# Kernel optimization log

Hardware: AMD Instinct MI355X
Metric: run time of the kernel (lower is better)

Reference implementation:

```python
import jax, jax.numpy as jnp
import numpy as np

INV_SCALE = 1.0 / (0.5 * 9)  # module's inv_scale_factor; qk is DIVIDED by this (i.e. * 4.5)


def setup_inputs() -> dict:
    key0 = jax.random.key(0)
    ks = jax.random.split(key0, 8)
    B, Sq, Sk, D, Dv = 8, 2048, 2048, 128, 256
    return {
        "query": jax.random.normal(ks[0], (B, Sq, D), dtype=jnp.float32),
        "key": jax.random.normal(ks[1], (B, Sk, D), dtype=jnp.float32),
        "value": jax.random.normal(ks[2], (B, Sk, Dv), dtype=jnp.float32),
        "mask": jax.random.normal(ks[3], (B, Sq, Sk), dtype=jnp.float32),
        # Linear weights stored torch-style as [out_features, in_features]
        "W0": jax.random.normal(ks[4], (D, D), dtype=jnp.float32) * (1.0 / np.sqrt(D)),
        "W1": jax.random.normal(ks[5], (D, D), dtype=jnp.float32) * (1.0 / np.sqrt(D)),
        "W2": jax.random.normal(ks[6], (D, Dv), dtype=jnp.float32) * (1.0 / np.sqrt(Dv)),
        "Wout": jax.random.normal(ks[7], (Dv, D), dtype=jnp.float32) * (1.0 / np.sqrt(D)),
    }


def reference(query, key, value, mask, W0, W1, W2, Wout):
    r1 = jnp.einsum("bqd,od->bqo", query, W0)          # [B,Sq,128]
    r2 = jnp.einsum("bkd,od->bko", key, W1)            # [B,Sk,128]
    r3 = jnp.einsum("bkv,ov->bko", value, W2)          # [B,Sk,128]
    qk = jnp.einsum("bqd,bkd->bqk", r1, r2)            # [B,Sq,Sk]
    scaled_qk = qk / INV_SCALE
    softmax_qk = jax.nn.softmax(scaled_qk, axis=-1)
    # dropout is identity in eval mode (deterministic reference)
    v1 = jnp.einsum("bqk,bko->bqo", softmax_qk, r3)    # [B,Sq,128]
    v2 = jnp.einsum("bqo,vo->bqv", v1, Wout)           # [B,Sq,256]
    output = v2 + jnp.einsum("bqk,bkv->bqv", mask, value)
    return output
```

## Files before the change

kernel.cpp:

```cpp
#include <hip/hip_runtime.h>
#include <cstdint>

typedef __attribute__((ext_vector_type(8))) __bf16 bf16x8;
typedef __attribute__((ext_vector_type(4))) __bf16 bf16x4;
typedef __attribute__((ext_vector_type(4))) float f32x4;

#define MFMA16(a, b, c) __builtin_amdgcn_mfma_f32_16x16x32_bf16((a), (b), (c), 0, 0, 0)
#define WAITV(N) asm volatile("s_waitcnt vmcnt(" #N ")" ::: "memory")

static constexpr int SEQ = 2048;
static constexpr int DV = 256;
static constexpr float QK_SCALE = 4.5f;

__device__ __forceinline__ bf16x4 cvt4(float4 v) {
    bf16x4 y;
    y[0] = (__bf16)v.x; y[1] = (__bf16)v.y; y[2] = (__bf16)v.z; y[3] = (__bf16)v.w;
    return y;
}

__device__ __forceinline__ void gl_lds16(const void* g, void* l) {
    __builtin_amdgcn_global_load_lds((const __attribute__((address_space(1))) uint32_t*)g,
                                     (__attribute__((address_space(3))) uint32_t*)l, 16, 0, 0);
}

template <int K, int TRANS>
__device__ __forceinline__ void proj_body(const float* __restrict__ X,
                                          const float* __restrict__ W,
                                          __bf16* __restrict__ out,
                                          float outScale, int m0, char* smem) {
    auto ldsX = (__bf16(*)[136])smem;
    auto ldsW = (__bf16(*)[136])(smem + 64 * 136 * 2);

    const int t = threadIdx.x;
    const int w = t >> 6, l = t & 63, lrow = l & 15, lq = l >> 4;

    f32x4 acc[8];
#pragma unroll
    for (int i = 0; i < 8; ++i) acc[i] = f32x4{0.f, 0.f, 0.f, 0.f};

#pragma unroll
    for (int kh = 0; kh < K / 128; ++kh) {
        if (kh) __syncthreads();
#pragma unroll
        for (int i = 0; i < 8; ++i) {
            int idx = t + i * 256;
            int r = idx >> 5, c4 = idx & 31;
            float4 v = *(const float4*)(X + (size_t)(m0 + r) * K + kh * 128 + c4 * 4);
            *(bf16x4*)&ldsX[r][c4 * 4] = cvt4(v);
        }
#pragma unroll
        for (int i = 0; i < 16; ++i) {
            int idx = t + i * 256;
            int r = idx >> 5, c4 = idx & 31;
            float4 v = *(const float4*)(W + (size_t)r * K + kh * 128 + c4 * 4);
            *(bf16x4*)&ldsW[r][c4 * 4] = cvt4(v);
        }
        __syncthreads();

        bf16x8 aA[4];
#pragma unroll
        for (int kc = 0; kc < 4; ++kc)
            aA[kc] = *(const bf16x8*)((const char*)&ldsX[w * 16 + lrow][0] + kc * 64 + lq * 16);
#pragma unroll
        for (int nt = 0; nt < 8; ++nt) {
#pragma unroll
            for (int kc = 0; kc < 4; ++kc) {
                bf16x8 bB = *(const bf16x8*)((const char*)&ldsW[nt * 16 + lrow][0] + kc * 64 + lq * 16);
                acc[nt] = MFMA16(aA[kc], bB, acc[nt]);
            }
        }
    }

#pragma unroll
    for (int nt = 0; nt < 8; ++nt) {
        if (TRANS) {
            int gm = m0 + w * 16 + lq * 4;
            int b = gm >> 11, s = gm & 2047;
            int col = nt * 16 + lrow;
            int kt = s >> 5, s32 = s & 31;
            int slot = (s32 >> 3) ^ ((col >> 1) & 3);
            bf16x4 y;
#pragma unroll
            for (int j = 0; j < 4; ++j) y[j] = (__bf16)(acc[nt][j] * outScale);
            *(bf16x4*)(out + (((size_t)b * 64 + kt) * 128 + col) * 32 + slot * 8 + (s32 & 7)) = y;
        } else {
#pragma unroll
            for (int j = 0; j < 4; ++j) {
                int gm = m0 + w * 16 + lq * 4 + j;
                int col = nt * 16 + lrow;
                out[(size_t)gm * 128 + col] = (__bf16)(acc[nt][j] * outScale);
            }
        }
    }
}

__device__ __forceinline__ void vt_body(const float* __restrict__ V,
                                        __bf16* __restrict__ vt, int wg, char* smem) {
    auto tile = (__bf16(*)[72])smem;
    const int t = threadIdx.x;
    const int b = wg >> 7, by = (wg >> 5) & 3, bxx = wg & 31;
    const int s0 = bxx * 64, v0 = by * 64;
#pragma unroll
    for (int i = 0; i < 4; ++i) {
        int idx = t + i * 256;
        int r = idx >> 4, c4 = idx & 15;
        float4 x = *(const float4*)(V + ((size_t)b * SEQ + s0 + r) * DV + v0 + c4 * 4);
        *(bf16x4*)&tile[r][c4 * 4] = cvt4(x);
    }
    __syncthreads();
#pragma unroll
    for (int i = 0; i < 4; ++i) {
        int idx = t + i * 256;
        int vv = idx >> 4, c4 = idx & 15;
        bf16x4 y;
        y[0] = tile[c4 * 4 + 0][vv]; y[1] = tile[c4 * 4 + 1][vv];
        y[2] = tile[c4 * 4 + 2][vv]; y[3] = tile[c4 * 4 + 3][vv];
        int v = v0 + vv;
        int kt = (s0 >> 5) + (c4 >> 3);
        int slot = ((c4 >> 1) & 3) ^ ((v >> 1) & 3);
        *(bf16x4*)(vt + (((size_t)b * 64 + kt) * 256 + v) * 32 + slot * 8 + (c4 & 1) * 4) = y;
    }
}

__global__ __launch_bounds__(256) void k_pre(const float* __restrict__ q,
                                             const float* __restrict__ k,
                                             const float* __restrict__ v,
                                             const float* __restrict__ W0,
                                             const float* __restrict__ W1,
                                             const float* __restrict__ W2,
                                             const float* __restrict__ Wout,
                                             __bf16* __restrict__ r1s,
                                             __bf16* __restrict__ r2b,
                                             __bf16* __restrict__ r3t,
                                             __bf16* __restrict__ vtb,
                                             __bf16* __restrict__ wob) {
    __shared__ __align__(16) char smem[52224];
    const int bx = blockIdx.x;
    if (bx < 256) {
        proj_body<128, 0>(q, W0, r1s, QK_SCALE, bx * 64, smem);
    } else if (bx < 512) {
        proj_body<128, 0>(k, W1, r2b, 1.0f, (bx - 256) * 64, smem);
    } else if (bx < 768) {
        proj_body<256, 1>(v, W2, r3t, 1.0f, (bx - 512) * 64, smem);
    } else if (bx < 1792) {
        vt_body(v, vtb, bx - 768, smem);
    } else {
        int i = (bx - 1792) * 256 + threadIdx.x;
        if (i < 8192) {
            float4 x = *(const float4*)(Wout + (size_t)i * 4);
            *(bf16x4*)(wob + (size_t)i * 4) = cvt4(x);
        }
    }
}

__global__ __launch_bounds__(256) void k_flash(const __bf16* __restrict__ r1s,
                                               const __bf16* __restrict__ r2,
                                               const __bf16* __restrict__ r3p,
                                               __bf16* __restrict__ v1p,
                                               float* __restrict__ ml) {
    __shared__ __align__(16) __bf16 r2s[4][32 * 128];
    __shared__ __align__(16) __bf16 r3s[4][128 * 32];
    __shared__ __bf16 plds[4][16][48];

    const int t = threadIdx.x;
    const int bx = (int)((blockIdx.x & 7) * 64 + (blockIdx.x >> 3));
    const int b = bx >> 6, rem = bx & 63, q0 = (rem >> 1) * 64, kh = rem & 1;
    const int w = t >> 6, l = t & 63, lrow = l & 15, lq = l >> 4;

    const __bf16* r1b = r1s + (size_t)b * SEQ * 128;
    const __bf16* r2b = r2 + (size_t)b * SEQ * 128 + (size_t)kh * 1024 * 128;
    const __bf16* r3b = r3p + (size_t)b * 64 * 128 * 32 + (size_t)kh * 32 * 128 * 32;

    bf16x8 aQ[4];
    {
        const __bf16* p = r1b + (size_t)(q0 + w * 16 + lrow) * 128 + lq * 8;
#pragma unroll
        for (int kc = 0; kc < 4; ++kc) aQ[kc] = *(const bf16x8*)(p + kc * 32);
    }

    const __bf16* p_r2[2];
    const __bf16* p_r3[2];
#pragma unroll
    for (int q1 = 0; q1 < 2; ++q1) {
        int r = 8 * w + 4 * q1 + (l >> 4);
        int c = (l & 15) ^ (r & 15);
        p_r2[q1] = r2b + (size_t)r * 128 + c * 8;
        p_r3[q1] = r3b + (size_t)(2 * w + q1) * 512 + l * 8;
    }

    auto stage = [&](int bi) {
#pragma unroll
        for (int q1 = 0; q1 < 2; ++q1) {
            gl_lds16(p_r2[q1], &r2s[bi][(2 * w + q1) * 512]);
            gl_lds16(p_r3[q1], &r3s[bi][(2 * w + q1) * 512]);
            p_r2[q1] += 32 * 128;
            p_r3[q1] += 128 * 32;
        }
    };

    f32x4 acc[8];
#pragma unroll
    for (int i = 0; i < 8; ++i) acc[i] = f32x4{0.f, 0.f, 0.f, 0.f};
    float mrow[4] = {-INFINITY, -INFINITY, -INFINITY, -INFINITY};
    float lsum[4] = {0.f, 0.f, 0.f, 0.f};

    stage(0); stage(1); stage(2);
    for (int it = 0; it < 32; ++it) {
        if (it < 30) { WAITV(8); } else if (it == 30) { WAITV(4); } else { WAITV(0); }
        __builtin_amdgcn_s_barrier();
        __builtin_amdgcn_sched_barrier(0);
        if (it + 3 < 32) stage((it + 3) & 3);
        __builtin_amdgcn_sched_barrier(0);
        const __bf16* R2 = &r2s[it & 3][0];
        const __bf16* R3 = &r3s[it & 3][0];

        f32x4 sc[2];
#pragma unroll
        for (int ct = 0; ct < 2; ++ct) {
            f32x4 s = f32x4{0.f, 0.f, 0.f, 0.f};
#pragma unroll
            for (int kc = 0; kc < 4; ++kc) {
                int p = (kc * 4 + lq) ^ lrow;
                bf16x8 bb = *(const bf16x8*)&R2[(ct * 16 + lrow) * 128 + p * 8];
                s = MFMA16(aQ[kc], bb, s);
            }
            sc[ct] = s;
        }

        float pm[4], al[4];
#pragma unroll
        for (int j = 0; j < 4; ++j) pm[j] = fmaxf(sc[0][j], sc[1][j]);
#pragma unroll
        for (int off = 1; off <= 8; off <<= 1)
#pragma unroll
            for (int j = 0; j < 4; ++j) pm[j] = fmaxf(pm[j], __shfl_xor(pm[j], off, 64));
#pragma unroll
        for (int j = 0; j < 4; ++j) {
            float mn = fmaxf(mrow[j], pm[j]);
            al[j] = __expf(mrow[j] - mn);
            mrow[j] = mn;
        }
        float pr[2][4];
#pragma unroll
        for (int ct = 0; ct < 2; ++ct)
#pragma unroll
            for (int j = 0; j < 4; ++j)
                pr[ct][j] = __expf(sc[ct][j] - mrow[j]);
#pragma unroll
        for (int j = 0; j < 4; ++j)
            lsum[j] = lsum[j] * al[j] + pr[0][j] + pr[1][j];
#pragma unroll
        for (int ot = 0; ot < 8; ++ot)
#pragma unroll
            for (int j = 0; j < 4; ++j) acc[ot][j] *= al[j];

#pragma unroll
        for (int ct = 0; ct < 2; ++ct)
#pragma unroll
            for (int j = 0; j < 4; ++j)
                plds[w][lq * 4 + j][ct * 16 + lrow] = (__bf16)pr[ct][j];
        __builtin_amdgcn_s_waitcnt(0xc07f);
        bf16x8 pA = *(const bf16x8*)&plds[w][lrow][lq * 8];

#pragma unroll
        for (int ot = 0; ot < 8; ++ot) {
            int p = lq ^ ((lrow >> 1) & 3);
            bf16x8 bb = *(const bf16x8*)&R3[(ot * 16 + lrow) * 32 + p * 8];
            acc[ot] = MFMA16(pA, bb, acc[ot]);
        }
    }

#pragma unroll
    for (int off = 1; off <= 8; off <<= 1)
#pragma unroll
        for (int j = 0; j < 4; ++j) lsum[j] += __shfl_xor(lsum[j], off, 64);

    __bf16* vp = v1p + (size_t)kh * 8 * SEQ * 128;
#pragma unroll
    for (int ot = 0; ot < 8; ++ot)
#pragma unroll
        for (int j = 0; j < 4; ++j) {
            int q = q0 + w * 16 + lq * 4 + j;
            float v = acc[ot][j] / lsum[j];
            vp[((size_t)b * SEQ + q) * 128 + ot * 16 + lrow] = (__bf16)v;
        }
    if (lrow == 0) {
#pragma unroll
        for (int j = 0; j < 4; ++j) {
            size_t row = (size_t)b * SEQ + q0 + w * 16 + lq * 4 + j;
            ml[((size_t)kh * 8 * SEQ + row) * 2 + 0] = mrow[j];
            ml[((size_t)kh * 8 * SEQ + row) * 2 + 1] = lsum[j];
        }
    }
}

__global__ __launch_bounds__(512, 4) void k_out(const float* __restrict__ mask,
                                                const __bf16* __restrict__ vtp,
                                                const __bf16* __restrict__ v1p,
                                                const float* __restrict__ ml,
                                                const __bf16* __restrict__ wob,
                                                float* __restrict__ out) {
    __shared__ __align__(16) __bf16 vbuf[3][256 * 32];
    __shared__ __align__(16) float mbuf[4][32 * 64];

    const int t = threadIdx.x;
    const int bid = (int)((blockIdx.x & 7) * 64 + (blockIdx.x >> 3));
    const int m0 = bid * 32;
    const int b = m0 >> 11, q0 = m0 & 2047;
    const int w = t >> 6, l = t & 63, lrow = l & 15, lq = l >> 4;
    const int rg = w & 1, cg = w >> 1;

    f32x4 acc[4];
#pragma unroll
    for (int i = 0; i < 4; ++i) acc[i] = f32x4{0.f, 0.f, 0.f, 0.f};

    const __bf16* vsrc[4];
    const float* msrc[2];
    if (w < 4) {
#pragma unroll
        for (int i = 0; i < 4; ++i)
            vsrc[i] = vtp + (size_t)b * 64 * 8192 + (w * 4 + i) * 512 + l * 8;
    } else {
        const int m = w - 4;
#pragma unroll
        for (int s = 0; s < 2; ++s) {
            int r = 4 * (m * 2 + s) + (l >> 4);
            int c = (l & 15) ^ (r & 7);
            msrc[s] = mask + ((size_t)(b * 2048 + q0 + r)) * 2048 + c * 4;
        }
    }

    if (w < 4) {
#pragma unroll
        for (int kt = 0; kt < 2; ++kt)
#pragma unroll
            for (int i = 0; i < 4; ++i)
                gl_lds16(vsrc[i] + (size_t)kt * 8192, &vbuf[kt][(w * 4 + i) * 512]);
    } else {
        const int m = w - 4;
#pragma unroll
        for (int e = 0; e < 2; ++e)
#pragma unroll
            for (int s = 0; s < 2; ++s)
                gl_lds16(msrc[s] + (size_t)e * 64, &mbuf[e][(m * 2 + s) * 256]);
    }

    for (int it = 0; it < 64; ++it) {
        if (w >= 4) {
            const int m = w - 4;
            if (it <= 59) {
                int en = (it >> 1) + 2, s = it & 1;
                gl_lds16(msrc[s] + (size_t)en * 64, &mbuf[en & 3][(m * 2 + s) * 256]);
            }
            if ((it & 1) == 0) {
                if (it <= 58) { WAITV(3); } else if (it == 60) { WAITV(2); } else { WAITV(0); }
            }
        } else {
            if (it < 63) { WAITV(4); } else { WAITV(0); }
        }
        __builtin_amdgcn_s_barrier();
        __builtin_amdgcn_sched_barrier(0);
        if (w < 4 && it + 2 < 64) {
            int kt = it + 2;
#pragma unroll
            for (int i = 0; i < 4; ++i)
                gl_lds16(vsrc[i] + (size_t)kt * 8192, &vbuf[kt % 3][(w * 4 + i) * 512]);
        }
        __builtin_amdgcn_sched_barrier(0);

        const float* Mb = &mbuf[(it >> 1) & 3][0];
        const __bf16* V = &vbuf[it % 3][0];
        const int h = it & 1;
        int c0 = (h * 8 + lq * 2) ^ (lrow & 7);
        int c1 = (h * 8 + lq * 2 + 1) ^ (lrow & 7);
        float4 f0 = *(const float4*)&Mb[(rg * 16 + lrow) * 64 + c0 * 4];
        float4 f1 = *(const float4*)&Mb[(rg * 16 + lrow) * 64 + c1 * 4];
        bf16x8 aM;
        aM[0] = (__bf16)f0.x; aM[1] = (__bf16)f0.y; aM[2] = (__bf16)f0.z; aM[3] = (__bf16)f0.w;
        aM[4] = (__bf16)f1.x; aM[5] = (__bf16)f1.y; aM[6] = (__bf16)f1.z; aM[7] = (__bf16)f1.w;

        const int pv = lq ^ ((lrow >> 1) & 3);
#pragma unroll
        for (int vt8 = 0; vt8 < 4; ++vt8) {
            bf16x8 bb = *(const bf16x8*)&V[(cg * 64 + vt8 * 16 + lrow) * 32 + pv * 8];
            acc[vt8] = MFMA16(aM, bb, acc[vt8]);
        }
    }

    const int NROW = 8 * SEQ;
    const int row = m0 + rg * 16 + lrow;
    float am0 = ml[(size_t)row * 2 + 0], al0 = ml[(size_t)row * 2 + 1];
    float am1 = ml[((size_t)NROW + row) * 2 + 0], al1 = ml[((size_t)NROW + row) * 2 + 1];
    float M = fmaxf(am0, am1);
    float w0 = al0 * __expf(am0 - M), w1 = al1 * __expf(am1 - M);
    float inv = 1.f / (w0 + w1);
    w0 *= inv; w1 *= inv;
    bf16x8 aV[4];
#pragma unroll
    for (int oc = 0; oc < 4; ++oc) {
        bf16x8 a = *(const bf16x8*)(v1p + (size_t)row * 128 + oc * 32 + lq * 8);
        bf16x8 bh = *(const bf16x8*)(v1p + ((size_t)NROW + row) * 128 + oc * 32 + lq * 8);
        bf16x8 o;
#pragma unroll
        for (int j = 0; j < 8; ++j) o[j] = (__bf16)((float)a[j] * w0 + (float)bh[j] * w1);
        aV[oc] = o;
    }
#pragma unroll
    for (int vt8 = 0; vt8 < 4; ++vt8) {
#pragma unroll
        for (int oc = 0; oc < 4; ++oc) {
            bf16x8 bb = *(const bf16x8*)(wob + (size_t)(cg * 64 + vt8 * 16 + lrow) * 128 + oc * 32 + lq * 8);
            acc[vt8] = MFMA16(aV[oc], bb, acc[vt8]);
        }
    }

#pragma unroll
    for (int vt8 = 0; vt8 < 4; ++vt8)
#pragma unroll
        for (int j = 0; j < 4; ++j) {
            int gq = m0 + rg * 16 + lq * 4 + j;
            out[(size_t)gq * 256 + cg * 64 + vt8 * 16 + lrow] = acc[vt8][j];
        }
}

extern "C" void kernel_launch(void* const* d_in, const int* in_sizes, int n_in,
                              void* d_out, int out_size, void* d_ws, size_t ws_size,
                              hipStream_t stream) {
    const float* q    = (const float*)d_in[0];
    const float* k    = (const float*)d_in[1];
    const float* v    = (const float*)d_in[2];
    const float* mask = (const float*)d_in[3];
    const float* W0   = (const float*)d_in[4];
    const float* W1   = (const float*)d_in[5];
    const float* W2   = (const float*)d_in[6];
    const float* Wout = (const float*)d_in[7];
    float* out = (float*)d_out;

    char* ws = (char*)d_ws;
    __bf16* r1s = (__bf16*)(ws);
    __bf16* r2b = (__bf16*)(ws + (4ull << 20));
    __bf16* r3t = (__bf16*)(ws + (8ull << 20));
    __bf16* vtb = (__bf16*)(ws + (12ull << 20));
    __bf16* wob = (__bf16*)(ws + (20ull << 20));
    __bf16* v1p = (__bf16*)(ws + (25ull << 20));
    float*  mlb = (float*)(ws + (33ull << 20));

    k_pre<<<1824, 256, 0, stream>>>(q, k, v, W0, W1, W2, Wout, r1s, r2b, r3t, vtb, wob);
    k_flash<<<512, 256, 0, stream>>>(r1s, r2b, r3t, v1p, mlb);
    k_out<<<512, 512, 0, stream>>>(mask, vtb, v1p, mlb, wob, out);
}
```

Before: 335.1 us.

## Pre-convert mask to bf16 in prep kernel and deepen V pipeline in output kernel

Adds a grid-stride section to the prep kernel that converts the full fp32 mask to bf16 in workspace. The output kernel then streams bf16 mask tiles into LDS and loads MFMA operands directly without per-iteration conversion, and the V tile ring grows from 3 to 4 stages with a prefetch distance of 3. The aim is to halve mask bytes and LDS use in the output GEMM and remove conversion ALU work. In exchange the mask is read in fp32 once and written and re-read in bf16, which adds total HBM traffic.

```diff
diff --git a/kernel.cpp b/kernel.cpp
--- a/kernel.cpp
+++ b/kernel.cpp
@@ -129,11 +129,13 @@
                                              const float* __restrict__ W1,
                                              const float* __restrict__ W2,
                                              const float* __restrict__ Wout,
+                                             const float* __restrict__ mask,
                                              __bf16* __restrict__ r1s,
                                              __bf16* __restrict__ r2b,
                                              __bf16* __restrict__ r3t,
                                              __bf16* __restrict__ vtb,
-                                             __bf16* __restrict__ wob) {
+                                             __bf16* __restrict__ wob,
+                                             __bf16* __restrict__ maskb) {
     __shared__ __align__(16) char smem[52224];
     const int bx = blockIdx.x;
     if (bx < 256) {
@@ -144,11 +146,23 @@
         proj_body<256, 1>(v, W2, r3t, 1.0f, (bx - 512) * 64, smem);
     } else if (bx < 1792) {
         vt_body(v, vtb, bx - 768, smem);
-    } else {
+    } else if (bx < 1824) {
         int i = (bx - 1792) * 256 + threadIdx.x;
         if (i < 8192) {
             float4 x = *(const float4*)(Wout + (size_t)i * 4);
             *(bf16x4*)(wob + (size_t)i * 4) = cvt4(x);
+        }
+    } else {
+        const size_t N = (size_t)8 * 2048 * 2048;
+        const size_t stride = (size_t)1024 * 256 * 8;
+        size_t i = ((size_t)(bx - 1824) * 256 + threadIdx.x) * 8;
+        for (; i < N; i += stride) {
+            float4 a = *(const float4*)(mask + i);
+            float4 b2 = *(const float4*)(mask + i + 4);
+            bf16x8 o;
+            o[0] = (__bf16)a.x; o[1] = (__bf16)a.y; o[2] = (__bf16)a.z; o[3] = (__bf16)a.w;
+            o[4] = (__bf16)b2.x; o[5] = (__bf16)b2.y; o[6] = (__bf16)b2.z; o[7] = (__bf16)b2.w;
+            *(bf16x8*)(maskb + i) = o;
         }
     }
 }
@@ -294,14 +308,14 @@
     }
 }
 
-__global__ __launch_bounds__(512, 4) void k_out(const float* __restrict__ mask,
+__global__ __launch_bounds__(512, 4) void k_out(const __bf16* __restrict__ maskb,
                                                 const __bf16* __restrict__ vtp,
                                                 const __bf16* __restrict__ v1p,
                                                 const float* __restrict__ ml,
                                                 const __bf16* __restrict__ wob,
                                                 float* __restrict__ out) {
-    __shared__ __align__(16) __bf16 vbuf[3][256 * 32];
-    __shared__ __align__(16) float mbuf[4][32 * 64];
+    __shared__ __align__(16) __bf16 vbuf[4][256 * 32];
+    __shared__ __align__(16) __bf16 mbuf[4][32 * 64];
 
     const int t = threadIdx.x;
     const int bid = (int)((blockIdx.x & 7) * 64 + (blockIdx.x >> 3));
@@ -315,24 +329,21 @@
     for (int i = 0; i < 4; ++i) acc[i] = f32x4{0.f, 0.f, 0.f, 0.f};
 
     const __bf16* vsrc[4];
-    const float* msrc[2];
+    const __bf16* msrc = nullptr;
     if (w < 4) {
 #pragma unroll
         for (int i = 0; i < 4; ++i)
             vsrc[i] = vtp + (size_t)b * 64 * 8192 + (w * 4 + i) * 512 + l * 8;
     } else {
         const int m = w - 4;
-#pragma unroll
-        for (int s = 0; s < 2; ++s) {
-            int r = 4 * (m * 2 + s) + (l >> 4);
-            int c = (l & 15) ^ (r & 7);
-            msrc[s] = mask + ((size_t)(b * 2048 + q0 + r)) * 2048 + c * 4;
-        }
+        int r = 8 * m + (l >> 3);
+        int c = (l & 7) ^ (l >> 3);
+        msrc = maskb + ((size_t)(b * 2048 + q0 + r)) * 2048 + c * 8;
     }
 
     if (w < 4) {
 #pragma unroll
-        for (int kt = 0; kt < 2; ++kt)
+        for (int kt = 0; kt < 3; ++kt)
 #pragma unroll
             for (int i = 0; i < 4; ++i)
                 gl_lds16(vsrc[i] + (size_t)kt * 8192, &vbuf[kt][(w * 4 + i) * 512]);
@@ -340,44 +351,34 @@
         const int m = w - 4;
 #pragma unroll
         for (int e = 0; e < 2; ++e)
-#pragma unroll
-            for (int s = 0; s < 2; ++s)
-                gl_lds16(msrc[s] + (size_t)e * 64, &mbuf[e][(m * 2 + s) * 256]);
+            gl_lds16(msrc + (size_t)e * 64, &mbuf[e][m * 512]);
     }
 
     for (int it = 0; it < 64; ++it) {
         if (w >= 4) {
             const int m = w - 4;
-            if (it <= 59) {
-                int en = (it >> 1) + 2, s = it & 1;
-                gl_lds16(msrc[s] + (size_t)en * 64, &mbuf[en & 3][(m * 2 + s) * 256]);
-            }
             if ((it & 1) == 0) {
-                if (it <= 58) { WAITV(3); } else if (it == 60) { WAITV(2); } else { WAITV(0); }
+                int en = (it >> 1) + 2;
+                if (en <= 31) gl_lds16(msrc + (size_t)en * 64, &mbuf[en & 3][m * 512]);
+                if (it <= 58) { WAITV(2); } else if (it == 60) { WAITV(1); } else { WAITV(0); }
             }
         } else {
-            if (it < 63) { WAITV(4); } else { WAITV(0); }
+            if (it <= 61) { WAITV(8); } else if (it == 62) { WAITV(4); } else { WAITV(0); }
         }
         __builtin_amdgcn_s_barrier();
         __builtin_amdgcn_sched_barrier(0);
-        if (w < 4 && it + 2 < 64) {
-            int kt = it + 2;
+        if (w < 4 && it + 3 < 64) {
+            int kt = it + 3;
 #pragma unroll
             for (int i = 0; i < 4; ++i)
-                gl_lds16(vsrc[i] + (size_t)kt * 8192, &vbuf[kt % 3][(w * 4 + i) * 512]);
+                gl_lds16(vsrc[i] + (size_t)kt * 8192, &vbuf[kt & 3][(w * 4 + i) * 512]);
         }
         __builtin_amdgcn_sched_barrier(0);
 
-        const float* Mb = &mbuf[(it >> 1) & 3][0];
-        const __bf16* V = &vbuf[it % 3][0];
+        const __bf16* Mb = &mbuf[(it >> 1) & 3][0];
+        const __bf16* V = &vbuf[it & 3][0];
         const int h = it & 1;
-        int c0 = (h * 8 + lq * 2) ^ (lrow & 7);
-        int c1 = (h * 8 + lq * 2 + 1) ^ (lrow & 7);
-        float4 f0 = *(const float4*)&Mb[(rg * 16 + lrow) * 64 + c0 * 4];
-        float4 f1 = *(const float4*)&Mb[(rg * 16 + lrow) * 64 + c1 * 4];
-        bf16x8 aM;
-        aM[0] = (__bf16)f0.x; aM[1] = (__bf16)f0.y; aM[2] = (__bf16)f0.z; aM[3] = (__bf16)f0.w;
-        aM[4] = (__bf16)f1.x; aM[5] = (__bf16)f1.y; aM[6] = (__bf16)f1.z; aM[7] = (__bf16)f1.w;
+        bf16x8 aM = *(const bf16x8*)&Mb[(rg * 16 + lrow) * 64 + (((h * 4 + lq) ^ (lrow & 7)) * 8)];
 
         const int pv = lq ^ ((lrow >> 1) & 3);
 #pragma unroll
@@ -444,8 +445,10 @@
     __bf16* wob = (__bf16*)(ws + (20ull << 20));
     __bf16* v1p = (__bf16*)(ws + (25ull << 20));
     float*  mlb = (float*)(ws + (33ull << 20));
-
-    k_pre<<<1824, 256, 0, stream>>>(q, k, v, W0, W1, W2, Wout, r1s, r2b, r3t, vtb, wob);
+    __bf16* mkb = (__bf16*)(ws + (34ull << 20));
+
+    k_pre<<<2848, 256, 0, stream>>>(q, k, v, W0, W1, W2, Wout, mask,
+                                    r1s, r2b, r3t, vtb, wob, mkb);
     k_flash<<<512, 256, 0, stream>>>(r1s, r2b, r3t, v1p, mlb);
-    k_out<<<512, 512, 0, stream>>>(mask, vtb, v1p, mlb, wob, out);
-}
+    k_out<<<512, 512, 0, stream>>>(mkb, vtb, v1p, mlb, wob, out);
+}
```

Result: no change. 339.5 us (+1.3%).
